# Performance work log

Hardware: AMD Instinct MI355X
Metric: run time of the kernel (lower is better)

## Reference

```python
import jax, jax.numpy as jnp
import numpy as np

N_POINTS = 262144
SP_FEAT = 128
HIDDEN = 64
EMBED = 256
NUM_SP = 4096
NUM_SP2 = 256
PAD_LIMIT = 64
MASK_RATIO = 0.6


def setup_inputs() -> dict:
    key = jax.random.key(0)
    ks = jax.random.split(key, 6)
    x = jax.random.normal(ks[0], (N_POINTS, SP_FEAT), jnp.float32)
    # point -> superpoint ids, sorted; force every superpoint non-empty
    idx10 = jax.random.randint(ks[1], (N_POINTS,), 0, NUM_SP)
    idx10 = jnp.sort(idx10.at[:NUM_SP].set(jnp.arange(NUM_SP))).astype(jnp.int32)
    # superpoint -> higher superpoint, balanced (16 per group, < PAD_LIMIT), sorted
    idx21 = ((jnp.arange(NUM_SP) * NUM_SP2) // NUM_SP).astype(jnp.int32)
    # deterministic mask: exactly int(NUM_SP * MASK_RATIO) superpoints masked
    mask_num = int(NUM_SP * MASK_RATIO)
    perm = jax.random.permutation(ks[2], NUM_SP)
    is_masked = jnp.zeros((NUM_SP,), bool).at[perm[:mask_num]].set(True)
    W1 = jax.random.normal(ks[3], (SP_FEAT, HIDDEN), jnp.float32) / np.sqrt(SP_FEAT).astype(np.float32)
    b1 = jnp.zeros((HIDDEN,), jnp.float32)
    W2 = jax.random.normal(ks[4], (HIDDEN, EMBED), jnp.float32) / np.sqrt(HIDDEN).astype(np.float32)
    b2 = jnp.zeros((EMBED,), jnp.float32)
    return {
        "full_features": x,
        "full_super_indices_10": idx10,
        "full_super_indices_21": idx21,
        "is_masked": is_masked,
        "W1": W1, "b1": b1, "W2": W2, "b2": b2,
    }


def _pad_scatter(tokens, idx21, flag):
    # tokens: [NUM_SP, C]; idx21 sorted sp->sp2 ids; flag: [NUM_SP] bool.
    # rank of each flagged superpoint within its sp2 group (in sp order)
    f = flag.astype(jnp.int32)
    cum = jnp.cumsum(f)                                            # inclusive global cumsum
    per_group = jax.ops.segment_sum(f, idx21, num_segments=NUM_SP2)
    prefix = jnp.concatenate([jnp.zeros((1,), jnp.int32), jnp.cumsum(per_group)[:-1]])
    rank = cum - 1 - prefix[idx21]                                 # 0-based slot within group
    slot = jnp.where(flag, rank, PAD_LIMIT)                        # PAD_LIMIT -> dropped
    out = jnp.zeros((NUM_SP2, PAD_LIMIT, tokens.shape[-1]), tokens.dtype)
    return out.at[idx21, slot].set(tokens, mode="drop")


def reference(full_features, full_super_indices_10, full_super_indices_21,
              is_masked, W1, b1, W2, b2):
    # per-point 2-layer MLP (gather is implicit: MLP is pointwise), then segment max
    h = jax.nn.relu(full_features @ W1 + b1)                       # [N, HIDDEN]
    h = jax.nn.relu(h @ W2 + b2)                                   # [N, EMBED]
    tok = jax.ops.segment_max(h, full_super_indices_10, num_segments=NUM_SP)  # [NUM_SP, EMBED]
    remain_tokens = _pad_scatter(tok, full_super_indices_21, ~is_masked)      # [NUM_SP2, PAD, EMBED]
    mask_tokens = _pad_scatter(tok, full_super_indices_21, is_masked)         # [NUM_SP2, PAD, EMBED]
    return (remain_tokens, mask_tokens)
```

## Files before the change

kernel.cpp:

```cpp
#include <hip/hip_runtime.h>
#include <hip/hip_bf16.h>

#define N_POINTS 262144
#define SP_FEAT 128
#define HIDDEN 64
#define EMBED 256
#define NUM_SP 4096
#define NUM_SP2 256
#define PAD_LIMIT 64
#define SLOTS 4
#define TILES 4
#define XS_STRIDE 136
#define H1_STRIDE 76
#define LOCAL_SP 8

typedef __bf16 bf16x8 __attribute__((ext_vector_type(8)));
typedef float floatx4 __attribute__((ext_vector_type(4)));
using bf16 = __hip_bfloat16;

__global__ __launch_bounds__(256) void fused_prep_kernel(
    const float* __restrict__ W1, const float* __restrict__ W2,
    const int* __restrict__ idx10, const int* __restrict__ idx21,
    const void* __restrict__ is_masked,
    bf16* __restrict__ W1t, bf16* __restrict__ W2t,
    int* __restrict__ start, int* __restrict__ invR, int* __restrict__ invM)
{
    const int tid = threadIdx.x;
    const int blk = blockIdx.x;

    if (blk < 256) {
        int p0 = (blk * 256 + tid) * 4;
        int4 v = *(const int4*)(idx10 + p0);
        if (p0 == 0) { start[0] = 0; start[NUM_SP] = N_POINTS; }
        if (v.y != v.x) start[v.y] = p0 + 1;
        if (v.z != v.y) start[v.z] = p0 + 2;
        if (v.w != v.z) start[v.w] = p0 + 3;
        if (p0 + 4 < N_POINTS) {
            int nx = idx10[p0 + 4];
            if (nx != v.w) start[nx] = p0 + 4;
        }
        return;
    }
    if (blk < 352) {
        int i = (blk - 256) * 256 + tid;
        if (i < HIDDEN * SP_FEAT) {
            int n = i >> 7, k = i & 127;
            W1t[i] = __float2bfloat16(W1[k * HIDDEN + n]);
        } else {
            int j = i - HIDDEN * SP_FEAT;
            int n = j >> 6, k = j & 63;
            W2t[j] = __float2bfloat16(W2[k * EMBED + n]);
        }
        return;
    }
    __shared__ int encS;
    if (tid == 0) encS = 0;
    __syncthreads();
    const unsigned char* mb = (const unsigned char*)is_masked;
    const int* mi = (const int*)is_masked;
    int local = 0;
    for (int p = tid; p < NUM_SP; p += 256)
        if ((p & 3) && mb[p]) local = 1;
    if (local) atomicOr(&encS, 1);
    __syncthreads();
    const int e = encS;

    const int g = tid;
    int a = 0, b = NUM_SP;
    while (a < b) { int m = (a + b) >> 1; if (idx21[m] < g) a = m + 1; else b = m; }
    int lo = a;
    b = NUM_SP;
    while (a < b) { int m = (a + b) >> 1; if (idx21[m] < g + 1) a = m + 1; else b = m; }
    int hi = a;
    int nR = 0, nM = 0;
    for (int s = lo; s < hi; ++s) {
        int msk = e ? (int)mb[s] : mi[s];
        if (msk) { if (nM < PAD_LIMIT) invM[g * PAD_LIMIT + nM] = s; nM++; }
        else     { if (nR < PAD_LIMIT) invR[g * PAD_LIMIT + nR] = s; nR++; }
    }
    for (int r = nR; r < PAD_LIMIT; ++r) invR[g * PAD_LIMIT + r] = -1;
    for (int r = nM; r < PAD_LIMIT; ++r) invM[g * PAD_LIMIT + r] = -1;
}

__global__ __launch_bounds__(256, 3) void mlp_segmax_kernel(
    const float* __restrict__ X, const int* __restrict__ idx10,
    const int* __restrict__ start,
    const bf16* __restrict__ W1t, const float* __restrict__ b1,
    const bf16* __restrict__ W2t, const float* __restrict__ b2,
    float* __restrict__ partial)
{
    __shared__ __align__(16) bf16 Xs[64][XS_STRIDE];
    __shared__ __align__(16) bf16 H1s[64][H1_STRIDE];
    __shared__ int tokL[LOCAL_SP][EMBED];
    __shared__ int sIdx[64];

    const int tid  = threadIdx.x;
    const int lane = tid & 63;
    const int w    = tid >> 6;
    const int l15  = lane & 15;
    const int quad = lane >> 4;
    const int blk  = blockIdx.x;

    const int srow = tid >> 4;
    const int scc  = (tid & 15) * 8;

    float4 u0[4], u1[4];
    {
        const float* src0 = X + (size_t)(blk * TILES * 64) * SP_FEAT;
#pragma unroll
        for (int i = 0; i < 4; ++i) {
            const float* src = src0 + (size_t)(srow + 16 * i) * SP_FEAT + scc;
            u0[i] = *(const float4*)src;
            u1[i] = *(const float4*)(src + 4);
        }
    }
    int i2 = 0;
    if (tid < 64) i2 = idx10[blk * TILES * 64 + tid];

#pragma unroll
    for (int j = 0; j < LOCAL_SP; ++j) tokL[j][tid] = 0;

    bf16x8 bf2[4][2];
#pragma unroll
    for (int tn = 0; tn < 4; ++tn) {
        const bf16* p = W2t + (64 * w + 16 * tn + l15) * HIDDEN + quad * 8;
#pragma unroll
        for (int ks = 0; ks < 2; ++ks) bf2[tn][ks] = *(const bf16x8*)(p + 32 * ks);
    }
    float b2f[4];
#pragma unroll
    for (int tn = 0; tn < 4; ++tn) b2f[tn] = b2[64 * w + 16 * tn + l15];
    const float b1v = b1[16 * w + l15];

    floatx4 zero4 = {0.f, 0.f, 0.f, 0.f};

    for (int t = 0; t < TILES; ++t) {
        const int bt = blk * TILES + t;
        const int m0 = bt * 64;

        if (tid < 64) sIdx[tid] = i2;

        bf16x8 bw1[4];
        {
            const bf16* p = W1t + (16 * w + l15) * SP_FEAT + quad * 8;
#pragma unroll
            for (int ks = 0; ks < 4; ++ks) bw1[ks] = *(const bf16x8*)(p + 32 * ks);
        }

#pragma unroll
        for (int i = 0; i < 4; ++i) {
            union { bf16x8 v; bf16 h[8]; } u;
            u.h[0] = __float2bfloat16(u0[i].x); u.h[1] = __float2bfloat16(u0[i].y);
            u.h[2] = __float2bfloat16(u0[i].z); u.h[3] = __float2bfloat16(u0[i].w);
            u.h[4] = __float2bfloat16(u1[i].x); u.h[5] = __float2bfloat16(u1[i].y);
            u.h[6] = __float2bfloat16(u1[i].z); u.h[7] = __float2bfloat16(u1[i].w);
            *(bf16x8*)(&Xs[srow + 16 * i][scc]) = u.v;
        }
        __syncthreads();

        if (t + 1 < TILES) {
            const float* src0 = X + (size_t)(m0 + 64) * SP_FEAT;
#pragma unroll
            for (int i = 0; i < 4; ++i) {
                const float* src = src0 + (size_t)(srow + 16 * i) * SP_FEAT + scc;
                u0[i] = *(const float4*)src;
                u1[i] = *(const float4*)(src + 4);
            }
            if (tid < 64) i2 = idx10[m0 + 64 + tid];
        }

        floatx4 acc1[4] = {zero4, zero4, zero4, zero4};
#pragma unroll
        for (int ks = 0; ks < 4; ++ks) {
            int k = ks * 32 + quad * 8;
#pragma unroll
            for (int tm = 0; tm < 4; ++tm) {
                bf16x8 a = *(bf16x8*)(&Xs[16 * tm + l15][k]);
                acc1[tm] = __builtin_amdgcn_mfma_f32_16x16x32_bf16(a, bw1[ks], acc1[tm], 0, 0, 0);
            }
        }
#pragma unroll
        for (int tm = 0; tm < 4; ++tm) {
#pragma unroll
            for (int r = 0; r < 4; ++r) {
                float v = acc1[tm][r] + b1v;
                v = v > 0.f ? v : 0.f;
                H1s[16 * tm + quad * 4 + r][16 * w + l15] = __float2bfloat16(v);
            }
        }
        __syncthreads();

        bf16x8 afr[4][2];
        int sps[16];
#pragma unroll
        for (int tm = 0; tm < 4; ++tm) {
            afr[tm][0] = *(bf16x8*)(&H1s[16 * tm + l15][quad * 8]);
            afr[tm][1] = *(bf16x8*)(&H1s[16 * tm + l15][32 + quad * 8]);
            int4 s4 = *(const int4*)(&sIdx[16 * tm + 4 * quad]);
            sps[4 * tm + 0] = s4.x; sps[4 * tm + 1] = s4.y;
            sps[4 * tm + 2] = s4.z; sps[4 * tm + 3] = s4.w;
        }
        const int sp0 = sIdx[0];

#pragma unroll
        for (int tn = 0; tn < 4; ++tn) {
            const int col = 64 * w + 16 * tn + l15;
            int cur_sp = -1;
            float cur = 0.f;
#pragma unroll
            for (int tm = 0; tm < 4; ++tm) {
                floatx4 acc = zero4;
                acc = __builtin_amdgcn_mfma_f32_16x16x32_bf16(afr[tm][0], bf2[tn][0], acc, 0, 0, 0);
                acc = __builtin_amdgcn_mfma_f32_16x16x32_bf16(afr[tm][1], bf2[tn][1], acc, 0, 0, 0);
#pragma unroll
                for (int r = 0; r < 4; ++r) {
                    float v = acc[r] + b2f[tn];
                    v = v > 0.f ? v : 0.f;
                    int sp = sps[4 * tm + r];
                    if (sp == cur_sp) {
                        cur = fmaxf(cur, v);
                    } else {
                        if (cur_sp >= 0) {
                            int local = cur_sp - sp0;
                            if (local < LOCAL_SP) {
                                atomicMax(&tokL[local][col], __float_as_int(cur));
                            } else {
                                int slot = bt - (start[cur_sp] >> 6);
                                atomicMax((int*)(partial + ((size_t)cur_sp * SLOTS +
                                          (slot < 3 ? slot : 3)) * EMBED + col),
                                          __float_as_int(cur));
                            }
                        }
                        cur_sp = sp;
                        cur = v;
                    }
                }
            }
            {
                int local = cur_sp - sp0;
                if (local < LOCAL_SP) {
                    atomicMax(&tokL[local][col], __float_as_int(cur));
                } else {
                    int slot = bt - (start[cur_sp] >> 6);
                    atomicMax((int*)(partial + ((size_t)cur_sp * SLOTS +
                              (slot < 3 ? slot : 3)) * EMBED + col),
                              __float_as_int(cur));
                }
            }
        }
        __syncthreads();

        int nsp = sIdx[63] - sp0 + 1;
        if (nsp > LOCAL_SP) nsp = LOCAL_SP;
        for (int j = 0; j < nsp; ++j) {
            int sp   = sp0 + j;
            int slot = bt - (start[sp] >> 6);
            int bits = tokL[j][tid];
            int* dst = (int*)(partial + ((size_t)sp * SLOTS + (slot < 3 ? slot : 3)) * EMBED + tid);
            if (slot < 3) *dst = bits;
            else atomicMax(dst, bits);
        }
#pragma unroll
        for (int j = 0; j < LOCAL_SP; ++j) tokL[j][tid] = 0;
        __syncthreads();
    }
}

__global__ __launch_bounds__(256) void scatter_kernel(
    const float4* __restrict__ partial4, const int* __restrict__ start,
    const int* __restrict__ invR, const int* __restrict__ invM,
    float4* __restrict__ out4)
{
    const int bb   = blockIdx.x;
    const int g    = bb & (NUM_SP2 - 1);
    const int slab = bb >> 8;
    const int tid  = threadIdx.x;
    const int c4   = tid & 63;
    const int r0   = tid >> 6;
    const int* tab = slab ? invM : invR;
    float4* o = out4 + ((size_t)slab * NUM_SP2 + g) * PAD_LIMIT * 64;
#pragma unroll 4
    for (int rr = 0; rr < 16; ++rr) {
        int row = r0 + rr * 4;
        int sp = tab[g * PAD_LIMIT + row];
        float4 v = {0.f, 0.f, 0.f, 0.f};
        if (sp >= 0) {
            int sb = start[sp] >> 6;
            int se = (start[sp + 1] - 1) >> 6;
            int ns = se - sb;
            const float4* p = partial4 + (size_t)sp * SLOTS * 64 + c4;
            v = p[0];
            if (ns > 0) {
                float4 q = p[64];
                v.x = fmaxf(v.x, q.x); v.y = fmaxf(v.y, q.y);
                v.z = fmaxf(v.z, q.z); v.w = fmaxf(v.w, q.w);
            }
            if (ns > 1) {
                float4 q = p[128];
                v.x = fmaxf(v.x, q.x); v.y = fmaxf(v.y, q.y);
                v.z = fmaxf(v.z, q.z); v.w = fmaxf(v.w, q.w);
            }
            if (ns > 2) {
                float4 q = p[192];
                v.x = fmaxf(v.x, q.x); v.y = fmaxf(v.y, q.y);
                v.z = fmaxf(v.z, q.z); v.w = fmaxf(v.w, q.w);
            }
        }
        o[row * 64 + c4] = v;
    }
}

extern "C" void kernel_launch(void* const* d_in, const int* in_sizes, int n_in,
                              void* d_out, int out_size, void* d_ws, size_t ws_size,
                              hipStream_t stream) {
    (void)in_sizes; (void)n_in; (void)ws_size; (void)out_size;
    const float* X        = (const float*)d_in[0];
    const int* idx10      = (const int*)d_in[1];
    const int* idx21      = (const int*)d_in[2];
    const void* is_masked = (const void*)d_in[3];
    const float* W1       = (const float*)d_in[4];
    const float* b1       = (const float*)d_in[5];
    const float* W2       = (const float*)d_in[6];
    const float* b2       = (const float*)d_in[7];

    char* ws       = (char*)d_ws;
    float* partial = (float*)ws;
    bf16* W1t      = (bf16*)(ws + (size_t)NUM_SP * SLOTS * EMBED * 4);
    bf16* W2t      = W1t + HIDDEN * SP_FEAT;
    int*  start    = (int*)((char*)(W2t + EMBED * HIDDEN));
    int*  invR     = start + (NUM_SP + 2);
    int*  invM     = invR + NUM_SP2 * PAD_LIMIT;

    fused_prep_kernel<<<353, 256, 0, stream>>>(
        W1, W2, idx10, idx21, is_masked, W1t, W2t, start, invR, invM);
    mlp_segmax_kernel<<<N_POINTS / (64 * TILES), 256, 0, stream>>>(
        X, idx10, start, W1t, b1, W2t, b2, partial);
    scatter_kernel<<<NUM_SP2 * 2, 256, 0, stream>>>(
        (const float4*)partial, start, invR, invM, (float4*)d_out);
}
```

Measured before the change: 260.0 us.

## Stage X tiles directly into swizzled LDS with global_load_lds

Input tiles are now copied from global memory straight into shared memory as fp32 using the direct global-to-LDS load, with an XOR swizzle to limit bank conflicts. The bf16 conversion moves to the point where MFMA operands are read. This removes the register staging buffers and frees VGPRs. The W1 fragments are hoisted out of the tile loop, and a barrier is dropped because each wave only touches its own token columns. In exchange, the fp32 tile doubles the LDS footprint, conversion is repeated on every operand read, and the next-tile prefetch is now issued later, during the second GEMM.

```diff
diff --git a/kernel.cpp b/kernel.cpp
--- a/kernel.cpp
+++ b/kernel.cpp
@@ -10,13 +10,27 @@
 #define PAD_LIMIT 64
 #define SLOTS 4
 #define TILES 4
-#define XS_STRIDE 136
 #define H1_STRIDE 76
 #define LOCAL_SP 8
 
 typedef __bf16 bf16x8 __attribute__((ext_vector_type(8)));
 typedef float floatx4 __attribute__((ext_vector_type(4)));
+typedef float f32x4 __attribute__((ext_vector_type(4)));
 using bf16 = __hip_bfloat16;
+
+#define GLDS16(gsrc, ldst)                                                  \
+    __builtin_amdgcn_global_load_lds(                                       \
+        (const __attribute__((address_space(1))) void*)(gsrc),              \
+        (__attribute__((address_space(3))) void*)(ldst), 16, 0, 0)
+
+static __device__ __forceinline__ bf16x8 cvt8(f32x4 a, f32x4 b) {
+    union { bf16x8 v; bf16 h[8]; } u;
+    u.h[0] = __float2bfloat16(a[0]); u.h[1] = __float2bfloat16(a[1]);
+    u.h[2] = __float2bfloat16(a[2]); u.h[3] = __float2bfloat16(a[3]);
+    u.h[4] = __float2bfloat16(b[0]); u.h[5] = __float2bfloat16(b[1]);
+    u.h[6] = __float2bfloat16(b[2]); u.h[7] = __float2bfloat16(b[3]);
+    return u.v;
+}
 
 __global__ __launch_bounds__(256) void fused_prep_kernel(
     const float* __restrict__ W1, const float* __restrict__ W2,
@@ -89,7 +103,7 @@
     const bf16* __restrict__ W2t, const float* __restrict__ b2,
     float* __restrict__ partial)
 {
-    __shared__ __align__(16) bf16 Xs[64][XS_STRIDE];
+    __shared__ __align__(16) float XsF[64 * SP_FEAT];
     __shared__ __align__(16) bf16 H1s[64][H1_STRIDE];
     __shared__ int tokL[LOCAL_SP][EMBED];
     __shared__ int sIdx[64];
@@ -101,25 +115,31 @@
     const int quad = lane >> 4;
     const int blk  = blockIdx.x;
 
-    const int srow = tid >> 4;
-    const int scc  = (tid & 15) * 8;
-
-    float4 u0[4], u1[4];
-    {
-        const float* src0 = X + (size_t)(blk * TILES * 64) * SP_FEAT;
-#pragma unroll
-        for (int i = 0; i < 4; ++i) {
-            const float* src = src0 + (size_t)(srow + 16 * i) * SP_FEAT + scc;
-            u0[i] = *(const float4*)src;
-            u1[i] = *(const float4*)(src + 4);
-        }
-    }
+    char* XsC = (char*)XsF;
+#define STAGE_TILE(m0)                                                       \
+    {                                                                        \
+        const char* gb = (const char*)(X + (size_t)(m0) * SP_FEAT);          \
+        _Pragma("unroll")                                                    \
+        for (int j = 0; j < 8; ++j) {                                        \
+            int o  = ((w * 8 + j) << 10) + lane * 16;                        \
+            int so = o ^ (((o >> 9) & 7) << 4);                              \
+            GLDS16(gb + so, XsC + ((w * 8 + j) << 10));                      \
+        }                                                                    \
+    }
+
+    STAGE_TILE(blk * TILES * 64);
     int i2 = 0;
     if (tid < 64) i2 = idx10[blk * TILES * 64 + tid];
-
 #pragma unroll
     for (int j = 0; j < LOCAL_SP; ++j) tokL[j][tid] = 0;
 
+    bf16x8 bw1[4];
+    {
+        const bf16* p = W1t + (16 * w + l15) * SP_FEAT + quad * 8;
+#pragma unroll
+        for (int ks = 0; ks < 4; ++ks) bw1[ks] = *(const bf16x8*)(p + 32 * ks);
+    }
+    const float b1v = b1[16 * w + l15];
     bf16x8 bf2[4][2];
 #pragma unroll
     for (int tn = 0; tn < 4; ++tn) {
@@ -130,7 +150,8 @@
     float b2f[4];
 #pragma unroll
     for (int tn = 0; tn < 4; ++tn) b2f[tn] = b2[64 * w + 16 * tn + l15];
-    const float b1v = b1[16 * w + l15];
+
+    __syncthreads();
 
     floatx4 zero4 = {0.f, 0.f, 0.f, 0.f};
 
@@ -140,42 +161,17 @@
 
         if (tid < 64) sIdx[tid] = i2;
 
-        bf16x8 bw1[4];
-        {
-            const bf16* p = W1t + (16 * w + l15) * SP_FEAT + quad * 8;
-#pragma unroll
-            for (int ks = 0; ks < 4; ++ks) bw1[ks] = *(const bf16x8*)(p + 32 * ks);
-        }
-
-#pragma unroll
-        for (int i = 0; i < 4; ++i) {
-            union { bf16x8 v; bf16 h[8]; } u;
-            u.h[0] = __float2bfloat16(u0[i].x); u.h[1] = __float2bfloat16(u0[i].y);
-            u.h[2] = __float2bfloat16(u0[i].z); u.h[3] = __float2bfloat16(u0[i].w);
-            u.h[4] = __float2bfloat16(u1[i].x); u.h[5] = __float2bfloat16(u1[i].y);
-            u.h[6] = __float2bfloat16(u1[i].z); u.h[7] = __float2bfloat16(u1[i].w);
-            *(bf16x8*)(&Xs[srow + 16 * i][scc]) = u.v;
-        }
-        __syncthreads();
-
-        if (t + 1 < TILES) {
-            const float* src0 = X + (size_t)(m0 + 64) * SP_FEAT;
-#pragma unroll
-            for (int i = 0; i < 4; ++i) {
-                const float* src = src0 + (size_t)(srow + 16 * i) * SP_FEAT + scc;
-                u0[i] = *(const float4*)src;
-                u1[i] = *(const float4*)(src + 4);
-            }
-            if (tid < 64) i2 = idx10[m0 + 64 + tid];
-        }
-
         floatx4 acc1[4] = {zero4, zero4, zero4, zero4};
 #pragma unroll
         for (int ks = 0; ks < 4; ++ks) {
-            int k = ks * 32 + quad * 8;
+            const int c0 = (32 * ks + 8 * quad) * 4;
 #pragma unroll
             for (int tm = 0; tm < 4; ++tm) {
-                bf16x8 a = *(bf16x8*)(&Xs[16 * tm + l15][k]);
+                const int rb = (16 * tm + l15) * 512;
+                const int s  = (l15 & 7) << 4;
+                f32x4 lo = *(const f32x4*)(XsC + (rb + ((c0) ^ s)));
+                f32x4 hi = *(const f32x4*)(XsC + (rb + ((c0 + 16) ^ s)));
+                bf16x8 a = cvt8(lo, hi);
                 acc1[tm] = __builtin_amdgcn_mfma_f32_16x16x32_bf16(a, bw1[ks], acc1[tm], 0, 0, 0);
             }
         }
@@ -189,6 +185,11 @@
             }
         }
         __syncthreads();
+
+        if (t + 1 < TILES) {
+            STAGE_TILE(m0 + 64);
+            if (tid < 64) i2 = idx10[m0 + 64 + tid];
+        }
 
         bf16x8 afr[4][2];
         int sps[16];
@@ -248,7 +249,6 @@
                 }
             }
         }
-        __syncthreads();
 
         int nsp = sIdx[63] - sp0 + 1;
         if (nsp > LOCAL_SP) nsp = LOCAL_SP;
@@ -264,6 +264,7 @@
         for (int j = 0; j < LOCAL_SP; ++j) tokL[j][tid] = 0;
         __syncthreads();
     }
+#undef STAGE_TILE
 }
 
 __global__ __launch_bounds__(256) void scatter_kernel(
```

Result: no change. 262.2 us (+0.9%).
